# Optimization experiments

Hardware: AMD Instinct MI355X
Metric: run time of the kernel (lower is better)

Reference implementation:

```python
import jax, jax.numpy as jnp
import numpy as np

N, E, G, H = 4096, 8192, 64, 128  # nodes, edges, graphs, hidden dim
NODE_DIM, EDGE_DIM = 11, 5


def _linear_params(key, fan_in, fan_out):
    kw, kb = jax.random.split(key)
    s = 1.0 / np.sqrt(fan_in)
    w = jax.random.uniform(kw, (fan_in, fan_out), minval=-s, maxval=s, dtype=jnp.float32)
    b = jax.random.uniform(kb, (fan_out,), minval=-s, maxval=s, dtype=jnp.float32)
    return w, b


def setup_inputs() -> dict:
    key = jax.random.key(0)
    ks = jax.random.split(key, 10)
    x = jax.random.normal(ks[0], (N, NODE_DIM), dtype=jnp.float32)
    edge_attr = jax.random.normal(ks[1], (E, EDGE_DIM), dtype=jnp.float32)
    edge_index = jax.random.randint(ks[2], (2, E), 0, N, dtype=jnp.int64)
    batch = jnp.sort(jax.random.randint(ks[3], (N,), 0, G, dtype=jnp.int64))
    # preprocess MLP: node_dim -> 128 -> 128
    p1_w, p1_b = _linear_params(ks[4], NODE_DIM, H)
    p2_w, p2_b = _linear_params(ks[5], H, H)
    # edge net: edge_dim -> 128 -> 256 -> 128 -> 128*128 (ReLU between, none after last)
    e1_w, e1_b = _linear_params(ks[6], EDGE_DIM, 128)
    e2_w, e2_b = _linear_params(ks[7], 128, 256)
    e3_w, e3_b = _linear_params(ks[8], 256, 128)
    e4_w, e4_b = _linear_params(ks[9], 128, H * H)
    return {"x": x, "edge_attr": edge_attr, "edge_index": edge_index, "batch": batch,
            "p1_w": p1_w, "p1_b": p1_b, "p2_w": p2_w, "p2_b": p2_b,
            "e1_w": e1_w, "e1_b": e1_b, "e2_w": e2_w, "e2_b": e2_b,
            "e3_w": e3_w, "e3_b": e3_b, "e4_w": e4_w, "e4_b": e4_b}


def reference(x, edge_attr, edge_index, batch,
              p1_w, p1_b, p2_w, p2_b,
              e1_w, e1_b, e2_w, e2_b, e3_w, e3_b, e4_w, e4_b):
    # node preprocess MLP (maps 11-dim features to 128 so NNConv dims are consistent)
    h = jax.nn.relu(x @ p1_w + p1_b) @ p2_w + p2_b  # [N, H]
    # edge network -> per-edge weight matrix [E, H, H]
    e = jax.nn.relu(edge_attr @ e1_w + e1_b)
    e = jax.nn.relu(e @ e2_w + e2_b)
    e = jax.nn.relu(e @ e3_w + e3_b)
    W = (e @ e4_w + e4_b).reshape(E, H, H)
    # NNConv (root_weight=False, bias=False, aggr='mean'):
    src, dst = edge_index[0], edge_index[1]
    msg = jnp.einsum('ei,eio->eo', h[src], W)  # gather + per-edge matmul, [E, H]
    agg = jax.ops.segment_sum(msg, dst, num_segments=N)
    cnt = jax.ops.segment_sum(jnp.ones((E,), msg.dtype), dst, num_segments=N)
    h_out = agg / jnp.maximum(cnt, 1.0)[:, None]  # scatter-mean, [N, H]
    # global add pool over graphs
    pooled = jax.ops.segment_sum(h_out, batch, num_segments=G)  # [G, H]
    return pooled
```

## Files before the change

kernel.cpp:

```cpp
#include <hip/hip_runtime.h>
#include <hip/hip_bf16.h>

#define N_NODES 4096
#define N_EDGES 8192
#define N_GRAPHS 64
#define HDIM 128

typedef __attribute__((ext_vector_type(8))) short bf16x8;
typedef __attribute__((ext_vector_type(4))) float f32x4;

static __device__ __forceinline__ unsigned short f2bf(float f) {
    unsigned u = __builtin_bit_cast(unsigned, f);
    u += 0x7fffu + ((u >> 16) & 1u);
    return (unsigned short)(u >> 16);
}
static __device__ __forceinline__ float bf2f(unsigned short s) {
    unsigned u = ((unsigned)s) << 16;
    return __builtin_bit_cast(float, u);
}

__global__ __launch_bounds__(256) void pre_kernel(
    const float* __restrict__ x, const float* __restrict__ p1w, const float* __restrict__ p1b,
    const float* __restrict__ p2w, const float* __restrict__ p2b, const float* __restrict__ e4b,
    unsigned short* __restrict__ h_bf, float* __restrict__ hb,
    const float* __restrict__ ea, const float* __restrict__ w1, const float* __restrict__ b1,
    const float* __restrict__ w4, unsigned short* __restrict__ w4perm,
    const float* __restrict__ w2, unsigned short* __restrict__ w2p,
    const float* __restrict__ w3, unsigned short* __restrict__ w3p,
    unsigned short* __restrict__ l1bf)
{
    __shared__ __align__(16) char smem[33024];
    const int t = threadIdx.x;
    const int bid = blockIdx.x;

    if (bid < 256) {
        float (*xs)[11]  = (float(*)[11])smem;
        float (*l1t)[16] = (float(*)[16])(smem + 704);
        float (*hs)[16]  = (float(*)[16])(smem + 8896);
        const int nb = bid;

        for (int r = t; r < 16 * 11; r += 256) {
            int e = r / 11, d = r % 11;
            xs[e][d] = x[(nb * 16 + e) * 11 + d];
        }
        __syncthreads();
        {
            int j = t & 127;
            float wd[11];
            #pragma unroll
            for (int d = 0; d < 11; ++d) wd[d] = p1w[d * 128 + j];
            float bj = p1b[j];
            for (int p = 0; p < 8; ++p) {
                int e = p * 2 + (t >> 7);
                float acc = bj;
                #pragma unroll
                for (int d = 0; d < 11; ++d) acc += xs[e][d] * wd[d];
                l1t[j][e] = fmaxf(acc, 0.f);
            }
        }
        __syncthreads();
        {
            int j = t & 127, eh = t >> 7;
            float acc[8];
            float bj = p2b[j];
            #pragma unroll
            for (int r = 0; r < 8; ++r) acc[r] = bj;
            for (int k = 0; k < 128; ++k) {
                float w = p2w[k * 128 + j];
                const float4* row = (const float4*)&l1t[k][eh * 8];
                float4 v0 = row[0], v1 = row[1];
                acc[0] += v0.x * w; acc[1] += v0.y * w; acc[2] += v0.z * w; acc[3] += v0.w * w;
                acc[4] += v1.x * w; acc[5] += v1.y * w; acc[6] += v1.z * w; acc[7] += v1.w * w;
            }
            #pragma unroll
            for (int r = 0; r < 8; ++r) {
                int e = eh * 8 + r;
                h_bf[(nb * 16 + e) * 128 + j] = f2bf(acc[r]);
                hs[j][e] = acc[r];
            }
        }
        __syncthreads();
        {
            int j = t & 127, eh = t >> 7;
            float acc[8] = {0.f,0.f,0.f,0.f,0.f,0.f,0.f,0.f};
            for (int i = 0; i < 128; ++i) {
                float w = e4b[i * 128 + j];
                const float4* row = (const float4*)&hs[i][eh * 8];
                float4 v0 = row[0], v1 = row[1];
                acc[0] += v0.x * w; acc[1] += v0.y * w; acc[2] += v0.z * w; acc[3] += v0.w * w;
                acc[4] += v1.x * w; acc[5] += v1.y * w; acc[6] += v1.z * w; acc[7] += v1.w * w;
            }
            #pragma unroll
            for (int r = 0; r < 8; ++r) hb[(nb * 16 + eh * 8 + r) * 128 + j] = acc[r];
        }
    } else if (bid < 384) {
        unsigned short (*tt)[129] = (unsigned short(*)[129])smem;
        const int i = bid - 256;
        for (int r = t; r < 16384; r += 256) {
            int k = r >> 7, o = r & 127;
            tt[o][k] = f2bf(w4[k * 16384 + i * 128 + o]);
        }
        __syncthreads();
        for (int r = t; r < 16384; r += 256) {
            int o = r >> 7, k = r & 127;
            w4perm[((size_t)(o >> 5) * 128 + i) * 4352 + (size_t)(o & 31) * 136 + k] = tt[o][k];
        }
    } else if (bid < 386) {
        unsigned short (*tt)[129] = (unsigned short(*)[129])smem;
        const int oh = bid - 384;
        for (int r = t; r < 16384; r += 256) {
            int k = r >> 7, ol = r & 127;
            tt[ol][k] = f2bf(w2[k * 256 + oh * 128 + ol]);
        }
        __syncthreads();
        for (int r = t; r < 16384; r += 256) {
            int ol = r >> 7, k = r & 127;
            w2p[(oh * 128 + ol) * 136 + k] = tt[ol][k];
        }
    } else if (bid < 388) {
        unsigned short (*tt)[257] = (unsigned short(*)[257])smem;
        const int oh = bid - 386;
        for (int r = t; r < 16384; r += 256) {
            int k = r >> 6, ol = r & 63;
            tt[ol][k] = f2bf(w3[k * 128 + oh * 64 + ol]);
        }
        __syncthreads();
        for (int r = t; r < 16384; r += 256) {
            int ol = r >> 8, k = r & 255;
            w3p[(oh * 64 + ol) * 264 + k] = tt[ol][k];
        }
    } else {
        float (*es)[5] = (float(*)[5])smem;
        const int eb = (bid - 388) * 256;
        for (int r = t; r < 1280; r += 256) ((float*)es)[r] = ea[eb * 5 + r];
        __syncthreads();
        int j = t & 127, eh = t >> 7;
        float wd[5];
        #pragma unroll
        for (int d = 0; d < 5; ++d) wd[d] = w1[d * 128 + j];
        float bj = b1[j];
        for (int p = 0; p < 128; ++p) {
            int e = eh * 128 + p;
            float acc = bj;
            #pragma unroll
            for (int d = 0; d < 5; ++d) acc += es[e][d] * wd[d];
            l1bf[(size_t)(eb + e) * 128 + j] = f2bf(fmaxf(acc, 0.f));
        }
    }
}

__global__ __launch_bounds__(256, 2) void edge23_kernel(
    const unsigned short* __restrict__ l1bf,
    const float* __restrict__ b2, const float* __restrict__ b3,
    const unsigned short* __restrict__ w2p, const unsigned short* __restrict__ w3p,
    unsigned short* __restrict__ e3bf)
{
    __shared__ __align__(16) unsigned short l2a[32 * 264];
    const int t = threadIdx.x, bid = blockIdx.x;
    const int w = t >> 6, lane = t & 63, q = lane >> 4, l15 = lane & 15;
    const int e0 = bid * 32;
    const f32x4 zero4 = (f32x4){0.f, 0.f, 0.f, 0.f};

    bf16x8 afrag[2][4];
    #pragma unroll
    for (int mb = 0; mb < 2; ++mb)
        #pragma unroll
        for (int s = 0; s < 4; ++s)
            afrag[mb][s] = *(const bf16x8*)(l1bf + (size_t)(e0 + mb * 16 + l15) * 128 + s * 32 + q * 8);

    f32x4 acc[2][4];
    #pragma unroll
    for (int mb = 0; mb < 2; ++mb)
        #pragma unroll
        for (int ob = 0; ob < 4; ++ob) acc[mb][ob] = zero4;
    #pragma unroll
    for (int ob = 0; ob < 4; ++ob) {
        const int o = w * 64 + ob * 16 + l15;
        bf16x8 bfrag[4];
        #pragma unroll
        for (int s = 0; s < 4; ++s)
            bfrag[s] = *(const bf16x8*)(w2p + (size_t)o * 136 + s * 32 + q * 8);
        #pragma unroll
        for (int mb = 0; mb < 2; ++mb) {
            f32x4 tmp = __builtin_amdgcn_mfma_f32_16x16x32_bf16(afrag[mb][0], bfrag[0], zero4, 0, 0, 0);
            tmp = __builtin_amdgcn_mfma_f32_16x16x32_bf16(afrag[mb][1], bfrag[1], tmp, 0, 0, 0);
            tmp = __builtin_amdgcn_mfma_f32_16x16x32_bf16(afrag[mb][2], bfrag[2], tmp, 0, 0, 0);
            acc[mb][ob] = __builtin_amdgcn_mfma_f32_16x16x32_bf16(afrag[mb][3], bfrag[3], tmp, 0, 0, 0);
        }
    }
    #pragma unroll
    for (int mb = 0; mb < 2; ++mb)
        #pragma unroll
        for (int ob = 0; ob < 4; ++ob) {
            int o = w * 64 + ob * 16 + l15;
            float bo = b2[o];
            #pragma unroll
            for (int r = 0; r < 4; ++r) {
                int e_loc = mb * 16 + q * 4 + r;
                l2a[e_loc * 264 + o] = f2bf(fmaxf(acc[mb][ob][r] + bo, 0.f));
            }
        }
    __syncthreads();

    f32x4 acc3[2][2];
    #pragma unroll
    for (int mb = 0; mb < 2; ++mb)
        #pragma unroll
        for (int ob = 0; ob < 2; ++ob) acc3[mb][ob] = zero4;
    #pragma unroll
    for (int ks = 0; ks < 8; ++ks) {
        bf16x8 a3[2];
        #pragma unroll
        for (int mb = 0; mb < 2; ++mb)
            a3[mb] = *(const bf16x8*)&l2a[(mb * 16 + l15) * 264 + ks * 32 + q * 8];
        #pragma unroll
        for (int ob = 0; ob < 2; ++ob) {
            const int o = w * 32 + ob * 16 + l15;
            bf16x8 bf = *(const bf16x8*)(w3p + (size_t)o * 264 + ks * 32 + q * 8);
            #pragma unroll
            for (int mb = 0; mb < 2; ++mb)
                acc3[mb][ob] = __builtin_amdgcn_mfma_f32_16x16x32_bf16(a3[mb], bf, acc3[mb][ob], 0, 0, 0);
        }
    }
    #pragma unroll
    for (int mb = 0; mb < 2; ++mb)
        #pragma unroll
        for (int ob = 0; ob < 2; ++ob) {
            int o = w * 32 + ob * 16 + l15;
            float bo = b3[o];
            #pragma unroll
            for (int r = 0; r < 4; ++r) {
                int e = e0 + mb * 16 + q * 4 + r;
                e3bf[(size_t)e * 128 + o] = f2bf(fmaxf(acc3[mb][ob][r] + bo, 0.f));
            }
        }
}

__global__ __launch_bounds__(256, 4) void nnconv_kernel(
    const unsigned short* __restrict__ e3bf, const unsigned short* __restrict__ h_bf,
    const unsigned short* __restrict__ w4perm, const float* __restrict__ hb,
    const int* __restrict__ ei, float* __restrict__ agg, float* __restrict__ cnt)
{
    __shared__ __align__(16) float ht_f[64 * 128];
    const int t = threadIdx.x;
    const int bid = blockIdx.x;
    const int osplit = bid & 7;
    const int ksplit = (bid >> 3) & 1;
    const int etile  = bid >> 4;
    const int w = t >> 6, lane = t & 63, q = lane >> 4, l15 = lane & 15;
    const int e0 = etile * 128;
    const int o0 = osplit * 16;
    const int i0 = ksplit * 64;

    bf16x8 afrag[2][4];
    #pragma unroll
    for (int mb = 0; mb < 2; ++mb)
        #pragma unroll
        for (int s = 0; s < 4; ++s) {
            int row = e0 + w * 32 + mb * 16 + l15;
            afrag[mb][s] = *(const bf16x8*)(e3bf + (size_t)row * 128 + s * 32 + q * 8);
        }

    {
        int r = t >> 1, part = t & 1;
        int s = ei[e0 + r];
        #pragma unroll
        for (int u = 0; u < 4; ++u) {
            uint4 v = *(const uint4*)(h_bf + (size_t)s * 128 + i0 + part * 32 + u * 8);
            const unsigned short* pv = (const unsigned short*)&v;
            #pragma unroll
            for (int j = 0; j < 8; ++j)
                ht_f[(part * 32 + u * 8 + j) * 128 + r] = bf2f(pv[j]);
        }
    }

    f32x4 acc[2];
    acc[0] = (f32x4){0.f, 0.f, 0.f, 0.f};
    acc[1] = (f32x4){0.f, 0.f, 0.f, 0.f};
    const f32x4 zero4 = (f32x4){0.f, 0.f, 0.f, 0.f};

    __syncthreads();

    const unsigned short* bbase =
        w4perm + ((size_t)(osplit >> 1) * 128 + i0) * 4352
               + (size_t)((osplit & 1) * 16 + l15) * 136 + q * 8;
    #pragma unroll 2
    for (int c = 0; c < 64; ++c) {
        const unsigned short* bp = bbase + (size_t)c * 4352;
        bf16x8 bfrag[4];
        #pragma unroll
        for (int s = 0; s < 4; ++s)
            bfrag[s] = *(const bf16x8*)(bp + s * 32);
        #pragma unroll
        for (int mb = 0; mb < 2; ++mb) {
            f32x4 hv = *(const f32x4*)&ht_f[c * 128 + w * 32 + mb * 16 + q * 4];
            f32x4 tmp = __builtin_amdgcn_mfma_f32_16x16x32_bf16(afrag[mb][0], bfrag[0], zero4, 0, 0, 0);
            tmp = __builtin_amdgcn_mfma_f32_16x16x32_bf16(afrag[mb][1], bfrag[1], tmp, 0, 0, 0);
            tmp = __builtin_amdgcn_mfma_f32_16x16x32_bf16(afrag[mb][2], bfrag[2], tmp, 0, 0, 0);
            tmp = __builtin_amdgcn_mfma_f32_16x16x32_bf16(afrag[mb][3], bfrag[3], tmp, 0, 0, 0);
            #pragma unroll
            for (int r = 0; r < 4; ++r)
                acc[mb][r] += hv[r] * tmp[r];
        }
    }

    #pragma unroll
    for (int mb = 0; mb < 2; ++mb) {
        #pragma unroll
        for (int r = 0; r < 4; ++r) {
            int e = e0 + w * 32 + mb * 16 + q * 4 + r;
            int de = ei[N_EDGES + e];
            int se = ei[e];
            if (osplit == 0 && ksplit == 0 && l15 == 0) atomicAdd(&cnt[de], 1.0f);
            int o = o0 + l15;
            float v = acc[mb][r];
            if (ksplit == 0) v += hb[(size_t)se * 128 + o];
            atomicAdd(&agg[(size_t)de * 128 + o], v);
        }
    }
}

__global__ __launch_bounds__(128) void pool_kernel(
    const float* __restrict__ agg, const float* __restrict__ cnt,
    const int* __restrict__ batch, float* __restrict__ out)
{
    const int g = blockIdx.x, t = threadIdx.x;
    int lo = 0, hi = N_NODES;
    while (lo < hi) { int m = (lo + hi) >> 1; if (batch[m] < g) lo = m + 1; else hi = m; }
    const int n_lo = lo;
    int lo2 = n_lo, hi2 = N_NODES;
    while (lo2 < hi2) { int m = (lo2 + hi2) >> 1; if (batch[m] < g + 1) lo2 = m + 1; else hi2 = m; }
    const int n_hi = lo2;

    float s0 = 0.f, s1 = 0.f, s2 = 0.f, s3 = 0.f;
    int n = n_lo;
    for (; n + 4 <= n_hi; n += 4) {
        float c0 = cnt[n], c1 = cnt[n + 1], c2 = cnt[n + 2], c3 = cnt[n + 3];
        float v0 = agg[(n    ) * 128 + t];
        float v1 = agg[(n + 1) * 128 + t];
        float v2 = agg[(n + 2) * 128 + t];
        float v3 = agg[(n + 3) * 128 + t];
        s0 += v0 / (c0 > 1.f ? c0 : 1.f);
        s1 += v1 / (c1 > 1.f ? c1 : 1.f);
        s2 += v2 / (c2 > 1.f ? c2 : 1.f);
        s3 += v3 / (c3 > 1.f ? c3 : 1.f);
    }
    for (; n < n_hi; ++n) {
        float c = cnt[n];
        s0 += agg[n * 128 + t] / (c > 1.f ? c : 1.f);
    }
    out[g * 128 + t] = (s0 + s1) + (s2 + s3);
}

extern "C" void kernel_launch(void* const* d_in, const int* in_sizes, int n_in,
                              void* d_out, int out_size, void* d_ws, size_t ws_size,
                              hipStream_t stream)
{
    const float* x     = (const float*)d_in[0];
    const float* ea    = (const float*)d_in[1];
    const int*   ei    = (const int*)d_in[2];
    const int*   batch = (const int*)d_in[3];
    const float* p1w   = (const float*)d_in[4];
    const float* p1b   = (const float*)d_in[5];
    const float* p2w   = (const float*)d_in[6];
    const float* p2b   = (const float*)d_in[7];
    const float* w1    = (const float*)d_in[8];
    const float* b1    = (const float*)d_in[9];
    const float* w2    = (const float*)d_in[10];
    const float* b2    = (const float*)d_in[11];
    const float* w3    = (const float*)d_in[12];
    const float* b3    = (const float*)d_in[13];
    const float* w4    = (const float*)d_in[14];
    const float* b4    = (const float*)d_in[15];
    float* out = (float*)d_out;
    (void)in_sizes; (void)n_in; (void)out_size; (void)ws_size;

    char* ws = (char*)d_ws;
    unsigned short* h_bf = (unsigned short*)(ws);
    unsigned short* e3bf = (unsigned short*)(ws + 1048576);
    float* hb            = (float*)(ws + 3145728);
    unsigned short* w4p  = (unsigned short*)(ws + 5242880);
    float* agg           = (float*)(ws + 9699328);
    unsigned short* l1bf = (unsigned short*)(ws + 9699328);
    float* cnt           = (float*)(ws + 11796480);
    unsigned short* w2p  = (unsigned short*)(ws + 11812864);
    unsigned short* w3p  = (unsigned short*)(ws + 11882496);

    pre_kernel<<<420, 256, 0, stream>>>(
        x, p1w, p1b, p2w, p2b, b4, h_bf, hb,
        ea, w1, b1, w4, w4p, w2, w2p, w3, w3p, l1bf);
    edge23_kernel<<<256, 256, 0, stream>>>(l1bf, b2, b3, w2p, w3p, e3bf);
    hipMemsetAsync(agg, 0, (size_t)N_NODES * 128 * 4 + (size_t)N_NODES * 4, stream);
    nnconv_kernel<<<1024, 256, 0, stream>>>(e3bf, h_bf, w4p, hb, ei, agg, cnt);
    pool_kernel<<<N_GRAPHS, 128, 0, stream>>>(agg, cnt, batch, out);
}
```

Before: 206.2 us.

## Retile NNConv to 64-edge tiles with intra-block k-split reduction, split layer-1 blocks

The NNConv kernel now processes 64 edges by 32 output columns per block instead of 128 edges by 16 columns. Its four waves split into two output groups and two k-halves, and the k-halves are combined through a shared-memory reduction before the atomic scatter. Each wave loads four A-fragment row blocks and reuses each W4 B-fragment across them, so the W4 reads per MFMA drop and each block issues fewer atomics. In exchange, register pressure rises (launch bounds lowered to 3 blocks per SIMD) and an extra barrier is added. Separately, the edge layer-1 part of pre_kernel handles 128 edges per block across more blocks, to spread that work wider.

```diff
diff --git a/kernel.cpp b/kernel.cpp
--- a/kernel.cpp
+++ b/kernel.cpp
@@ -131,16 +131,16 @@
         }
     } else {
         float (*es)[5] = (float(*)[5])smem;
-        const int eb = (bid - 388) * 256;
-        for (int r = t; r < 1280; r += 256) ((float*)es)[r] = ea[eb * 5 + r];
+        const int eb = (bid - 388) * 128;
+        for (int r = t; r < 640; r += 256) ((float*)es)[r] = ea[eb * 5 + r];
         __syncthreads();
         int j = t & 127, eh = t >> 7;
         float wd[5];
         #pragma unroll
         for (int d = 0; d < 5; ++d) wd[d] = w1[d * 128 + j];
         float bj = b1[j];
-        for (int p = 0; p < 128; ++p) {
-            int e = eh * 128 + p;
+        for (int p = 0; p < 64; ++p) {
+            int e = eh * 64 + p;
             float acc = bj;
             #pragma unroll
             for (int d = 0; d < 5; ++d) acc += es[e][d] * wd[d];
@@ -236,64 +236,73 @@
         }
 }
 
-__global__ __launch_bounds__(256, 4) void nnconv_kernel(
+__global__ __launch_bounds__(256, 3) void nnconv_kernel(
     const unsigned short* __restrict__ e3bf, const unsigned short* __restrict__ h_bf,
     const unsigned short* __restrict__ w4perm, const float* __restrict__ hb,
     const int* __restrict__ ei, float* __restrict__ agg, float* __restrict__ cnt)
 {
-    __shared__ __align__(16) float ht_f[64 * 128];
+    __shared__ __align__(16) float ht_f[64 * 64];
+    __shared__ __align__(16) float red[2 * 64 * 16];
     const int t = threadIdx.x;
     const int bid = blockIdx.x;
-    const int osplit = bid & 7;
-    const int ksplit = (bid >> 3) & 1;
-    const int etile  = bid >> 4;
+    const int osplit = bid & 3;
+    const int ksplit = (bid >> 2) & 1;
+    const int etile  = bid >> 3;
     const int w = t >> 6, lane = t & 63, q = lane >> 4, l15 = lane & 15;
-    const int e0 = etile * 128;
-    const int o0 = osplit * 16;
+    const int og   = w & 1;
+    const int kpar = w >> 1;
+    const int e0 = etile * 64;
+    const int o0 = osplit * 32;
     const int i0 = ksplit * 64;
 
-    bf16x8 afrag[2][4];
-    #pragma unroll
-    for (int mb = 0; mb < 2; ++mb)
+    bf16x8 afrag[4][4];
+    #pragma unroll
+    for (int mb = 0; mb < 4; ++mb)
         #pragma unroll
         for (int s = 0; s < 4; ++s) {
-            int row = e0 + w * 32 + mb * 16 + l15;
+            int row = e0 + mb * 16 + l15;
             afrag[mb][s] = *(const bf16x8*)(e3bf + (size_t)row * 128 + s * 32 + q * 8);
         }
+    #pragma unroll
+    for (int mb = 0; mb < 4; ++mb)
+        #pragma unroll
+        for (int s = 0; s < 4; ++s)
+            asm volatile("" : "+v"(afrag[mb][s]));
 
     {
-        int r = t >> 1, part = t & 1;
+        int r = t >> 2, part = t & 3;
         int s = ei[e0 + r];
         #pragma unroll
-        for (int u = 0; u < 4; ++u) {
-            uint4 v = *(const uint4*)(h_bf + (size_t)s * 128 + i0 + part * 32 + u * 8);
+        for (int u = 0; u < 2; ++u) {
+            uint4 v = *(const uint4*)(h_bf + (size_t)s * 128 + i0 + part * 16 + u * 8);
             const unsigned short* pv = (const unsigned short*)&v;
             #pragma unroll
             for (int j = 0; j < 8; ++j)
-                ht_f[(part * 32 + u * 8 + j) * 128 + r] = bf2f(pv[j]);
-        }
-    }
-
-    f32x4 acc[2];
-    acc[0] = (f32x4){0.f, 0.f, 0.f, 0.f};
-    acc[1] = (f32x4){0.f, 0.f, 0.f, 0.f};
+                ht_f[(part * 16 + u * 8 + j) * 64 + r] = bf2f(pv[j]);
+        }
+    }
+
+    f32x4 acc[4];
+    #pragma unroll
+    for (int mb = 0; mb < 4; ++mb) acc[mb] = (f32x4){0.f, 0.f, 0.f, 0.f};
     const f32x4 zero4 = (f32x4){0.f, 0.f, 0.f, 0.f};
 
     __syncthreads();
 
     const unsigned short* bbase =
-        w4perm + ((size_t)(osplit >> 1) * 128 + i0) * 4352
-               + (size_t)((osplit & 1) * 16 + l15) * 136 + q * 8;
+        w4perm + ((size_t)osplit * 128 + i0 + kpar * 32) * 4352
+               + (size_t)(og * 16 + l15) * 136 + q * 8;
     #pragma unroll 2
-    for (int c = 0; c < 64; ++c) {
+    for (int c = 0; c < 32; ++c) {
         const unsigned short* bp = bbase + (size_t)c * 4352;
         bf16x8 bfrag[4];
         #pragma unroll
         for (int s = 0; s < 4; ++s)
             bfrag[s] = *(const bf16x8*)(bp + s * 32);
-        #pragma unroll
-        for (int mb = 0; mb < 2; ++mb) {
-            f32x4 hv = *(const f32x4*)&ht_f[c * 128 + w * 32 + mb * 16 + q * 4];
+        const int cg = kpar * 32 + c;
+        #pragma unroll
+        for (int mb = 0; mb < 4; ++mb) {
+            f32x4 hv = *(const f32x4*)&ht_f[cg * 64 + mb * 16 + q * 4];
             f32x4 tmp = __builtin_amdgcn_mfma_f32_16x16x32_bf16(afrag[mb][0], bfrag[0], zero4, 0, 0, 0);
             tmp = __builtin_amdgcn_mfma_f32_16x16x32_bf16(afrag[mb][1], bfrag[1], tmp, 0, 0, 0);
             tmp = __builtin_amdgcn_mfma_f32_16x16x32_bf16(afrag[mb][2], bfrag[2], tmp, 0, 0, 0);
@@ -304,18 +313,30 @@
         }
     }
 
-    #pragma unroll
-    for (int mb = 0; mb < 2; ++mb) {
-        #pragma unroll
-        for (int r = 0; r < 4; ++r) {
-            int e = e0 + w * 32 + mb * 16 + q * 4 + r;
-            int de = ei[N_EDGES + e];
-            int se = ei[e];
-            if (osplit == 0 && ksplit == 0 && l15 == 0) atomicAdd(&cnt[de], 1.0f);
-            int o = o0 + l15;
-            float v = acc[mb][r];
-            if (ksplit == 0) v += hb[(size_t)se * 128 + o];
-            atomicAdd(&agg[(size_t)de * 128 + o], v);
+    if (kpar == 1) {
+        #pragma unroll
+        for (int mb = 0; mb < 4; ++mb)
+            #pragma unroll
+            for (int r = 0; r < 4; ++r)
+                red[(og * 64 + mb * 16 + q * 4 + r) * 16 + l15] = acc[mb][r];
+    }
+    __syncthreads();
+    if (kpar == 0) {
+        #pragma unroll
+        for (int mb = 0; mb < 4; ++mb) {
+            #pragma unroll
+            for (int r = 0; r < 4; ++r) {
+                int e_loc = mb * 16 + q * 4 + r;
+                int e = e0 + e_loc;
+                int de = ei[N_EDGES + e];
+                int se = ei[e];
+                int o = o0 + og * 16 + l15;
+                float v = acc[mb][r] + red[(og * 64 + e_loc) * 16 + l15];
+                if (ksplit == 0) v += hb[(size_t)se * 128 + o];
+                if (osplit == 0 && ksplit == 0 && og == 0 && l15 == 0)
+                    atomicAdd(&cnt[de], 1.0f);
+                atomicAdd(&agg[(size_t)de * 128 + o], v);
+            }
         }
     }
 }
@@ -386,7 +407,7 @@
     unsigned short* w2p  = (unsigned short*)(ws + 11812864);
     unsigned short* w3p  = (unsigned short*)(ws + 11882496);
 
-    pre_kernel<<<420, 256, 0, stream>>>(
+    pre_kernel<<<452, 256, 0, stream>>>(
         x, p1w, p1b, p2w, p2b, b4, h_bf, hb,
         ea, w1, b1, w4, w4p, w2, w2p, w3, w3p, l1bf);
     edge23_kernel<<<256, 256, 0, stream>>>(l1bf, b2, b3, w2p, w3p, e3bf);
```

Result: faster. 179.5 us (-13.0%).
